# Performance work log

Measured on AMD Instinct MI355X. Metric: run time of the kernel, lower is better.

Reference implementation:

```python
import jax, jax.numpy as jnp
import numpy as np

THETA = 128.0


def _make_Q(d, units):
    # Q[n,m] = (2n+1)/sqrt(d) if n > m and (n+m) odd, else 0 (fixed, non-trainable)
    n = np.arange(d)[:, None]
    m = np.arange(units)[None, :]
    Q = np.where((n > m) & (((n + m) % 2) == 1), (2 * n + 1) / np.sqrt(d), 0.0)
    return jnp.asarray(Q, dtype=jnp.float32)


def setup_inputs() -> dict:
    key = jax.random.key(0)
    k1, k2, k3, k4 = jax.random.split(key, 4)
    B_, T, Din, d, units = 16, 4096, 128, 256, 256
    x = jax.random.normal(k1, (B_, T, Din), dtype=jnp.float32)
    A = jax.random.normal(k2, (d, d), dtype=jnp.float32) / np.sqrt(d)
    Bm = jax.random.normal(k3, (Din, d), dtype=jnp.float32) / np.sqrt(Din)
    W_mix = jax.random.normal(k4, (units, units), dtype=jnp.float32) / np.sqrt(units)
    b_mix = jnp.zeros((units,), dtype=jnp.float32)
    return {"x": x, "A": A, "B": Bm, "W_mix": W_mix, "b_mix": b_mix}


def reference(x, A, B, W_mix, b_mix):
    d = A.shape[0]
    units = W_mix.shape[0]
    Q = _make_Q(d, units)
    QW = Q @ W_mix  # fuse fixed projection with dense kernel: (d, units)
    alpha = 1.0 - 1.0 / THETA
    beta = 1.0 / THETA
    # precompute input projection for all steps: (T, batch, d)
    xB = jnp.einsum('bti,id->tbd', x, B)

    def step(state, xBt):
        new_state = alpha * state + beta * (state @ A + xBt)
        y = jnp.tanh(new_state @ QW + b_mix)
        return new_state, y

    s0 = jnp.zeros((x.shape[0], d), dtype=x.dtype)
    _, ys = jax.lax.scan(step, s0, xB)  # ys: (T, batch, units)
    return jnp.transpose(ys, (1, 0, 2))
```

## Files before the change

### kernel.cpp

```cpp
#include <hip/hip_runtime.h>
#include <math.h>

constexpr int T_   = 4096;
constexpr int NB   = 16;
constexpr int D_   = 256;
constexpr int DIN  = 128;
constexpr int U_   = 256;
constexpr int L1   = 8;
constexpr int C1   = T_ / L1;
constexpr float ALPHA_ = 1.0f - 1.0f / 128.0f;
constexpr float BETA_  = 1.0f / 128.0f;
constexpr int SD   = NB * D_;
constexpr int MS   = D_ * D_;
constexpr int TLP  = D_ + 4;
constexpr int XLP  = DIN + 4;

using short8  = __attribute__((ext_vector_type(8))) short;
using float4v = __attribute__((ext_vector_type(4))) float;

__device__ __forceinline__ unsigned short bf16_rne(float x) {
  const unsigned b = __float_as_uint(x);
  const unsigned r = ((b >> 16) & 1u) + 0x7FFFu;
  return (unsigned short)((b + r) >> 16);
}
__device__ __forceinline__ float bf16_f(unsigned short h) {
  return __uint_as_float(((unsigned)h) << 16);
}

__device__ __forceinline__ void split2(float e0, float e1, unsigned& hd, unsigned& ld) {
  const unsigned b0 = __float_as_uint(e0), b1 = __float_as_uint(e1);
  const unsigned h0 = b0 & 0xFFFF0000u, h1 = b1 & 0xFFFF0000u;
  const float l0 = e0 - __uint_as_float(h0);
  const float l1 = e1 - __uint_as_float(h1);
  hd = (h0 >> 16) | h1;
  ld = (__float_as_uint(l0) >> 16) | (__float_as_uint(l1) & 0xFFFF0000u);
}

__device__ __forceinline__ void unpack8(uint4 a, uint4 b, short8& hi, short8& lo) {
  union { short8 s; unsigned u[4]; } H, L;
  const unsigned d[8] = {a.x, a.y, a.z, a.w, b.x, b.y, b.z, b.w};
#pragma unroll
  for (int i = 0; i < 4; ++i) {
    H.u[i] = (d[2 * i] >> 16) | (d[2 * i + 1] & 0xFFFF0000u);
    L.u[i] = (d[2 * i] & 0xFFFFu) | (d[2 * i + 1] << 16);
  }
  hi = H.s; lo = L.s;
}

__device__ __forceinline__ void mm_row(const float* __restrict__ Am,
                                       const float* __restrict__ Bm,
                                       float* __restrict__ Dm,
                                       int i, int tid, float* srow) {
  srow[tid] = Am[i * D_ + tid];
  __syncthreads();
  float a0 = 0.f, a1 = 0.f, a2 = 0.f, a3 = 0.f;
#pragma unroll 8
  for (int k = 0; k < D_; k += 4) {
    a0 = fmaf(srow[k + 0], Bm[(k + 0) * D_ + tid], a0);
    a1 = fmaf(srow[k + 1], Bm[(k + 1) * D_ + tid], a1);
    a2 = fmaf(srow[k + 2], Bm[(k + 2) * D_ + tid], a2);
    a3 = fmaf(srow[k + 3], Bm[(k + 3) * D_ + tid], a3);
  }
  Dm[i * D_ + tid] = (a0 + a1) + (a2 + a3);
  __syncthreads();
}

__global__ __launch_bounds__(256) void k_prep(const float* __restrict__ A,
                                              const float* __restrict__ W,
                                              float* __restrict__ Meff,
                                              float* __restrict__ QW) {
  const int bid = blockIdx.x, tid = threadIdx.x;
  if (bid < D_) {
    float v = BETA_ * A[bid * D_ + tid];
    if (bid == tid) v += ALPHA_;
    Meff[bid * D_ + tid] = v;
    return;
  }
  __shared__ float wch[32 * D_];
  float se = 0.f, so = 0.f;
  for (int ch = 0; ch < D_ / 32; ++ch) {
    __syncthreads();
    for (int idx = tid; idx < 32 * D_; idx += 256)
      wch[idx] = W[ch * 32 * D_ + idx];
    __syncthreads();
#pragma unroll
    for (int r = 0; r < 32; ++r) {
      const int n = ch * 32 + r;
      const float sum = (n & 1) ? se : so;
      QW[n * U_ + tid] = sum * ((float)(2 * n + 1) / 16.0f);
      const float wv = wch[r * D_ + tid];
      if (n & 1) so += wv; else se += wv;
    }
  }
}

__global__ __launch_bounds__(256) void k_pw(const float* __restrict__ Am,
                                            const float* __restrict__ Bbase,
                                            float* __restrict__ Dbase) {
  __shared__ float srow[D_];
  const int q = blockIdx.x >> 8, row = blockIdx.x & 255;
  mm_row(Am, Bbase + (size_t)q * MS, Dbase + (size_t)q * MS, row, threadIdx.x, srow);
}

__global__ __launch_bounds__(256) void k_pwr(const float* __restrict__ Abase,
                                             const float* __restrict__ Bm,
                                             float* __restrict__ Dbase) {
  __shared__ float srow[D_];
  const int q = blockIdx.x >> 8, row = blockIdx.x & 255;
  mm_row(Abase + (size_t)q * MS, Bm, Dbase + (size_t)q * MS, row, threadIdx.x, srow);
}

__global__ __launch_bounds__(256) void k_packA(const float* __restrict__ A,
                                               const float* __restrict__ Bm,
                                               unsigned short* __restrict__ Mf,
                                               unsigned short* __restrict__ Bmf) {
  const int bid = blockIdx.x, tid = threadIdx.x;
  const int lane = tid & 63, nb0 = tid >> 6;
  const int quad = lane >> 4, m16 = lane & 15;
  if (bid < 8) {
    const int ks = bid;
    for (int nb = nb0; nb < 16; nb += 4) {
      const size_t fo = ((size_t)(nb * 8 + ks) * 64 + lane) * 8;
#pragma unroll
      for (int jj = 0; jj < 8; ++jj) {
        const int k = ks * 32 + quad * 8 + jj;
        const int n = nb * 16 + m16;
        const float v = BETA_ * A[k * D_ + n];
        const unsigned short h = bf16_rne(v);
        Mf[fo + jj] = h;
        Mf[MS + fo + jj] = bf16_rne(v - bf16_f(h));
      }
    }
  } else {
    const int ks = bid - 8;
    unsigned short* dh = Bmf;
    unsigned short* dl = Bmf + (MS / 2);
    for (int nb = nb0; nb < 16; nb += 4) {
      const size_t fo = ((size_t)(nb * 4 + ks) * 64 + lane) * 8;
#pragma unroll
      for (int jj = 0; jj < 8; ++jj) {
        const int k = ks * 32 + quad * 8 + jj;
        const int n = nb * 16 + m16;
        const float v = BETA_ * Bm[k * D_ + n];
        const unsigned short h = bf16_rne(v);
        dh[fo + jj] = h;
        dl[fo + jj] = bf16_rne(v - bf16_f(h));
      }
    }
  }
}

__global__ __launch_bounds__(256) void k_packB(const float* __restrict__ R,
                                               const float* __restrict__ QWm,
                                               const float* __restrict__ M8,
                                               unsigned short* __restrict__ Bf,
                                               unsigned short* __restrict__ Pf0) {
  const int bid = blockIdx.x;
  const int mat = bid >> 3, ks = bid & 7;
  const float* X = (mat < 8) ? (R + (size_t)mat * MS) : (mat == 8 ? QWm : M8);
  unsigned short* dh = (mat < 9) ? (Bf + (size_t)mat * (2 * MS)) : Pf0;
  unsigned short* dl = dh + MS;
  const int tid = threadIdx.x, lane = tid & 63, nb0 = tid >> 6;
  const int quad = lane >> 4, m16 = lane & 15;
  for (int nb = nb0; nb < 16; nb += 4) {
    const size_t fo = ((size_t)(nb * 8 + ks) * 64 + lane) * 8;
#pragma unroll
    for (int jj = 0; jj < 8; ++jj) {
      const int k = ks * 32 + quad * 8 + jj;
      const int n = nb * 16 + m16;
      const float xv = X[k * D_ + n];
      const unsigned short h = bf16_rne(xv);
      dh[fo + jj] = h;
      dl[fo + jj] = bf16_rne(xv - bf16_f(h));
    }
  }
}

__global__ __launch_bounds__(256, 2) void k_passA(
    const float* __restrict__ x, const unsigned short* __restrict__ Bmf,
    const unsigned short* __restrict__ Mf,
    unsigned short* __restrict__ Shi, unsigned short* __restrict__ Slo,
    float* __restrict__ Ends) {
  __shared__ __align__(16) float xls[NB][XLP];
  __shared__ __align__(16) unsigned tls[NB][TLP];
  const int c = blockIdx.x, tid = threadIdx.x;
  const int w = tid >> 6, lane = tid & 63;
  const int m16 = lane & 15, q = lane >> 4;
  const int xrow = tid >> 4, xi0 = (tid & 15) * 8;

  float4v sC[4];
#pragma unroll
  for (int nt = 0; nt < 4; ++nt) sC[nt] = (float4v){0.f, 0.f, 0.f, 0.f};

  for (int j = 0; j < L1; ++j) {
    const int t = c * L1 + j;
    __syncthreads();
    {
      const float* xr = x + ((size_t)xrow * T_ + t) * DIN + xi0;
      const float4 v0 = *(const float4*)(xr);
      const float4 v1 = *(const float4*)(xr + 4);
      *(float4*)(&xls[xrow][xi0]) = v0;
      *(float4*)(&xls[xrow][xi0 + 4]) = v1;
    }
    if (j > 0) {
#pragma unroll
      for (int nt = 0; nt < 4; ++nt) {
        const int n = (w * 4 + nt) * 16 + m16;
#pragma unroll
        for (int r = 0; r < 4; ++r) {
          const float sv = sC[nt][r];
          const unsigned hb = __float_as_uint(sv) & 0xFFFF0000u;
          const float lo = sv - __uint_as_float(hb);
          tls[4 * q + r][n] = hb | (__float_as_uint(lo) >> 16);
        }
      }
    }
    __syncthreads();
    float4v acc[4];
#pragma unroll
    for (int nt = 0; nt < 4; ++nt) {
      acc[nt][0] = ALPHA_ * sC[nt][0];
      acc[nt][1] = ALPHA_ * sC[nt][1];
      acc[nt][2] = ALPHA_ * sC[nt][2];
      acc[nt][3] = ALPHA_ * sC[nt][3];
    }
#pragma unroll
    for (int ks = 0; ks < 4; ++ks) {
      float xv[8];
      *(float4*)(xv)     = *(const float4*)(&xls[m16][32 * ks + 8 * q]);
      *(float4*)(xv + 4) = *(const float4*)(&xls[m16][32 * ks + 8 * q + 4]);
      union { short8 s; unsigned u[4]; } XH, XL;
#pragma unroll
      for (int p = 0; p < 4; ++p) split2(xv[2 * p], xv[2 * p + 1], XH.u[p], XL.u[p]);
#pragma unroll
      for (int nt = 0; nt < 4; ++nt) {
        const size_t fo = ((size_t)((w * 4 + nt) * 4 + ks) * 64 + lane) * 8;
        const short8 bh = *(const short8*)(Bmf + fo);
        const short8 bl = *(const short8*)(Bmf + (MS / 2) + fo);
        acc[nt] = __builtin_amdgcn_mfma_f32_16x16x32_bf16(XH.s, bh, acc[nt], 0, 0, 0);
        acc[nt] = __builtin_amdgcn_mfma_f32_16x16x32_bf16(XH.s, bl, acc[nt], 0, 0, 0);
        acc[nt] = __builtin_amdgcn_mfma_f32_16x16x32_bf16(XL.s, bh, acc[nt], 0, 0, 0);
      }
    }
    if (j > 0) {
#pragma unroll
      for (int ks = 0; ks < 8; ++ks) {
        const uint4 p0 = *(const uint4*)(&tls[m16][32 * ks + 8 * q]);
        const uint4 p1 = *(const uint4*)(&tls[m16][32 * ks + 8 * q + 4]);
        short8 sh, sl; unpack8(p0, p1, sh, sl);
        const size_t ao = ((size_t)((t - 1) * 8 + ks) * 64 + lane) * 8;
        *(short8*)(Shi + ao) = sh;
        *(short8*)(Slo + ao) = sl;
#pragma unroll
        for (int nt = 0; nt < 4; ++nt) {
          const size_t fo = ((size_t)((w * 4 + nt) * 8 + ks) * 64 + lane) * 8;
          const short8 mh = *(const short8*)(Mf + fo);
          const short8 ml = *(const short8*)(Mf + MS + fo);
          acc[nt] = __builtin_amdgcn_mfma_f32_16x16x32_bf16(sh, mh, acc[nt], 0, 0, 0);
          acc[nt] = __builtin_amdgcn_mfma_f32_16x16x32_bf16(sh, ml, acc[nt], 0, 0, 0);
          acc[nt] = __builtin_amdgcn_mfma_f32_16x16x32_bf16(sl, mh, acc[nt], 0, 0, 0);
        }
      }
    }
#pragma unroll
    for (int nt = 0; nt < 4; ++nt) sC[nt] = acc[nt];
  }
  const int tl = c * L1 + L1 - 1;
  __syncthreads();
#pragma unroll
  for (int nt = 0; nt < 4; ++nt) {
    const int n = (w * 4 + nt) * 16 + m16;
#pragma unroll
    for (int r = 0; r < 4; ++r) {
      const float sv = sC[nt][r];
      const unsigned hb = __float_as_uint(sv) & 0xFFFF0000u;
      const float lo = sv - __uint_as_float(hb);
      tls[4 * q + r][n] = hb | (__float_as_uint(lo) >> 16);
    }
  }
  __syncthreads();
#pragma unroll
  for (int ks = 0; ks < 8; ++ks) {
    const uint4 p0 = *(const uint4*)(&tls[m16][32 * ks + 8 * q]);
    const uint4 p1 = *(const uint4*)(&tls[m16][32 * ks + 8 * q + 4]);
    short8 sh, sl; unpack8(p0, p1, sh, sl);
    const size_t ao = ((size_t)(tl * 8 + ks) * 64 + lane) * 8;
    *(short8*)(Shi + ao) = sh;
    *(short8*)(Slo + ao) = sl;
  }
#pragma unroll
  for (int nt = 0; nt < 4; ++nt) {
    const int n = (w * 4 + nt) * 16 + m16;
#pragma unroll
    for (int r = 0; r < 4; ++r)
      Ends[(size_t)c * SD + (size_t)(4 * q + r) * D_ + n] = sC[nt][r];
  }
}

__global__ __launch_bounds__(256) void k_scan(
    const float* __restrict__ Vin, float* __restrict__ Vout,
    const unsigned short* __restrict__ Pf,
    const float* __restrict__ Pf32,
    float* __restrict__ Psq,
    unsigned short* __restrict__ PfNext,
    int shift, int do_sq, int packmode,
    unsigned short* __restrict__ Hhi, unsigned short* __restrict__ Hlo) {
  __shared__ __align__(16) float smem[16 * TLP];
  const int bid = blockIdx.x, tid = threadIdx.x;
  if (bid >= C1) {
    if (!do_sq) return;
    const int i = bid - C1;
    smem[tid] = Pf32[i * D_ + tid];
    __syncthreads();
    float a0 = 0.f, a1 = 0.f, a2 = 0.f, a3 = 0.f;
#pragma unroll 8
    for (int k = 0; k < D_; k += 4) {
      a0 = fmaf(smem[k + 0], Pf32[(k + 0) * D_ + tid], a0);
      a1 = fmaf(smem[k + 1], Pf32[(k + 1) * D_ + tid], a1);
      a2 = fmaf(smem[k + 2], Pf32[(k + 2) * D_ + tid], a2);
      a3 = fmaf(smem[k + 3], Pf32[(k + 3) * D_ + tid], a3);
    }
    const float v = (a0 + a1) + (a2 + a3);
    Psq[i * D_ + tid] = v;
    const unsigned short h = bf16_rne(v);
    const unsigned short l = bf16_rne(v - bf16_f(h));
    const size_t off = ((size_t)((tid >> 4) * 8 + (i >> 5)) * 64 +
                        ((i >> 3) & 3) * 16 + (tid & 15)) * 8 + (i & 7);
    PfNext[off] = h;
    PfNext[MS + off] = l;
    return;
  }
  const int c = bid;
  const int w = tid >> 6, lane = tid & 63;
  const int m16 = lane & 15, q = lane >> 4;
  float4v acc[4];
#pragma unroll
  for (int nt = 0; nt < 4; ++nt) {
    const int n = (w * 4 + nt) * 16 + m16;
#pragma unroll
    for (int r = 0; r < 4; ++r)
      acc[nt][r] = Vin[(size_t)c * SD + (size_t)(4 * q + r) * D_ + n];
  }
  if (c >= shift) {
    const float* src = Vin + (size_t)(c - shift) * SD;
    {
      const int row = tid >> 4, col0 = (tid & 15) * 16;
#pragma unroll
      for (int p = 0; p < 4; ++p)
        *(float4*)(&smem[row * TLP + col0 + 4 * p]) =
            *(const float4*)(src + (size_t)row * D_ + col0 + 4 * p);
    }
    __syncthreads();
#pragma unroll
    for (int ks = 0; ks < 8; ++ks) {
      float xv[8];
      *(float4*)(xv)     = *(const float4*)(&smem[m16 * TLP + 32 * ks + 8 * q]);
      *(float4*)(xv + 4) = *(const float4*)(&smem[m16 * TLP + 32 * ks + 8 * q + 4]);
      union { short8 s; unsigned u[4]; } XH, XL;
#pragma unroll
      for (int p = 0; p < 4; ++p) split2(xv[2 * p], xv[2 * p + 1], XH.u[p], XL.u[p]);
#pragma unroll
      for (int nt = 0; nt < 4; ++nt) {
        const size_t fo = ((size_t)((w * 4 + nt) * 8 + ks) * 64 + lane) * 8;
        const short8 ph = *(const short8*)(Pf + fo);
        const short8 pl = *(const short8*)(Pf + MS + fo);
        acc[nt] = __builtin_amdgcn_mfma_f32_16x16x32_bf16(XH.s, ph, acc[nt], 0, 0, 0);
        acc[nt] = __builtin_amdgcn_mfma_f32_16x16x32_bf16(XH.s, pl, acc[nt], 0, 0, 0);
        acc[nt] = __builtin_amdgcn_mfma_f32_16x16x32_bf16(XL.s, ph, acc[nt], 0, 0, 0);
      }
    }
  }
  if (packmode) {
    __syncthreads();
    unsigned* tls = (unsigned*)smem;
#pragma unroll
    for (int nt = 0; nt < 4; ++nt) {
      const int n = (w * 4 + nt) * 16 + m16;
#pragma unroll
      for (int r = 0; r < 4; ++r) {
        const float sv = acc[nt][r];
        const unsigned hb = __float_as_uint(sv) & 0xFFFF0000u;
        const float lo = sv - __uint_as_float(hb);
        tls[(4 * q + r) * TLP + n] = hb | (__float_as_uint(lo) >> 16);
      }
    }
    __syncthreads();
#pragma unroll
    for (int ks = 0; ks < 8; ++ks) {
      const uint4 p0 = *(const uint4*)(&tls[m16 * TLP + 32 * ks + 8 * q]);
      const uint4 p1 = *(const uint4*)(&tls[m16 * TLP + 32 * ks + 8 * q + 4]);
      short8 sh, sl; unpack8(p0, p1, sh, sl);
      const size_t ao = ((size_t)(c * 8 + ks) * 64 + lane) * 8;
      *(short8*)(Hhi + ao) = sh;
      *(short8*)(Hlo + ao) = sl;
    }
  } else {
#pragma unroll
    for (int nt = 0; nt < 4; ++nt) {
      const int n = (w * 4 + nt) * 16 + m16;
#pragma unroll
      for (int r = 0; r < 4; ++r)
        Vout[(size_t)c * SD + (size_t)(4 * q + r) * D_ + n] = acc[nt][r];
    }
  }
}

__global__ __launch_bounds__(256, 2) void k_passB(
    const unsigned short* __restrict__ Shi, const unsigned short* __restrict__ Slo,
    const unsigned short* __restrict__ Hhi, const unsigned short* __restrict__ Hlo,
    const unsigned short* __restrict__ Bf, const float* __restrict__ bmix,
    float* __restrict__ out) {
  const int bid = blockIdx.x;
  const int g = bid >> 3, j = bid & 7;
  const int tid = threadIdx.x;
  const int w = tid >> 6, lane = tid & 63;
  const int m16 = lane & 15, quad = lane >> 4;
  const unsigned short* Qh = Bf + (size_t)8 * 2 * MS;
  const unsigned short* Ql = Qh + MS;
  const unsigned short* Rh = Bf + (size_t)j * 2 * MS;
  const unsigned short* Rl = Rh + MS;

  float4v acc[8][4];
#pragma unroll
  for (int ci = 0; ci < 8; ++ci)
#pragma unroll
    for (int nt = 0; nt < 4; ++nt) acc[ci][nt] = (float4v){0.f, 0.f, 0.f, 0.f};

  for (int ks = 0; ks < 8; ++ks) {
    short8 qh[4], ql[4], rh[4], rl[4];
#pragma unroll
    for (int nt = 0; nt < 4; ++nt) {
      const size_t fo = ((size_t)((w * 4 + nt) * 8 + ks) * 64 + lane) * 8;
      qh[nt] = *(const short8*)(Qh + fo);
      ql[nt] = *(const short8*)(Ql + fo);
      rh[nt] = *(const short8*)(Rh + fo);
      rl[nt] = *(const short8*)(Rl + fo);
    }
#pragma unroll
    for (int ci = 0; ci < 8; ++ci) {
      const int c = g * 8 + ci;
      const int t = c * 8 + j;
      const size_t ao = ((size_t)(t * 8 + ks) * 64 + lane) * 8;
      const short8 sh = *(const short8*)(Shi + ao);
      const short8 sl = *(const short8*)(Slo + ao);
#pragma unroll
      for (int nt = 0; nt < 4; ++nt) {
        float4v a = acc[ci][nt];
        a = __builtin_amdgcn_mfma_f32_16x16x32_bf16(sh, qh[nt], a, 0, 0, 0);
        a = __builtin_amdgcn_mfma_f32_16x16x32_bf16(sh, ql[nt], a, 0, 0, 0);
        a = __builtin_amdgcn_mfma_f32_16x16x32_bf16(sl, qh[nt], a, 0, 0, 0);
        acc[ci][nt] = a;
      }
      if (c > 0) {
        const size_t ho = ((size_t)((c - 1) * 8 + ks) * 64 + lane) * 8;
        const short8 hh = *(const short8*)(Hhi + ho);
        const short8 hl = *(const short8*)(Hlo + ho);
#pragma unroll
        for (int nt = 0; nt < 4; ++nt) {
          float4v a = acc[ci][nt];
          a = __builtin_amdgcn_mfma_f32_16x16x32_bf16(hh, rh[nt], a, 0, 0, 0);
          a = __builtin_amdgcn_mfma_f32_16x16x32_bf16(hh, rl[nt], a, 0, 0, 0);
          a = __builtin_amdgcn_mfma_f32_16x16x32_bf16(hl, rh[nt], a, 0, 0, 0);
          acc[ci][nt] = a;
        }
      }
    }
  }
  __shared__ float ysm[16][U_ + 4];
  for (int ci = 0; ci < 8; ++ci) {
    const int t = (g * 8 + ci) * 8 + j;
    __syncthreads();
#pragma unroll
    for (int nt = 0; nt < 4; ++nt) {
      const int n = (w * 4 + nt) * 16 + m16;
      const float bias = bmix[n];
#pragma unroll
      for (int r = 0; r < 4; ++r) {
        const float v = acc[ci][nt][r] + bias;
        const float e = __expf(2.0f * v);
        ysm[quad * 4 + r][n] = 1.0f - 2.0f / (e + 1.0f);
      }
    }
    __syncthreads();
    for (int idx = tid; idx < 16 * (U_ / 4); idx += 256) {
      const int b = idx >> 6, c4 = (idx & 63) * 4;
      const float4 v = make_float4(ysm[b][c4], ysm[b][c4 + 1],
                                   ysm[b][c4 + 2], ysm[b][c4 + 3]);
      *(float4*)(out + ((size_t)b * T_ + t) * U_ + c4) = v;
    }
  }
}

extern "C" void kernel_launch(void* const* d_in, const int* in_sizes, int n_in,
                              void* d_out, int out_size, void* d_ws, size_t ws_size,
                              hipStream_t stream) {
  const float* x    = (const float*)d_in[0];
  const float* A    = (const float*)d_in[1];
  const float* Bm   = (const float*)d_in[2];
  const float* W    = (const float*)d_in[3];
  const float* bmix = (const float*)d_in[4];
  float* out = (float*)d_out;

  float* ws = (float*)d_ws;
  unsigned short* Shi = (unsigned short*)ws;
  unsigned short* Slo = (unsigned short*)(ws + 8388608);
  float* pw  = ws + 16777216;
  float* QW  = pw + 8 * (size_t)MS;
  float* R   = QW + MS;
  float* Sa  = R + 8 * (size_t)MS;
  float* Sb  = Sa + MS;
  unsigned short* Bf  = (unsigned short*)(Sb + MS);
  unsigned short* Mf  = Bf + (size_t)9 * 2 * MS;
  unsigned short* Bmf = Mf + 2 * (size_t)MS;
  unsigned short* Pf0 = Bmf + MS;
  unsigned short* Pf1 = Pf0 + 2 * (size_t)MS;
  (void)in_sizes; (void)n_in; (void)out_size; (void)ws_size;

  float* Va = out;
  float* Vb = out + (size_t)C1 * SD;

  unsigned short* Hhi = (unsigned short*)d_in[0];
  unsigned short* Hlo = Hhi + (size_t)C1 * 16 * 256;

  k_prep<<<D_ + 1, 256, 0, stream>>>(A, W, pw, QW);
  k_packA<<<12, 256, 0, stream>>>(A, Bm, Mf, Bmf);
  k_passA<<<C1, 256, 0, stream>>>(x, Bmf, Mf, Shi, Slo, Va);
  k_pw<<<256, 256, 0, stream>>>(pw, pw, pw + MS);
  k_pw<<<512, 256, 0, stream>>>(pw + MS, pw, pw + 2 * (size_t)MS);
  k_pw<<<1024, 256, 0, stream>>>(pw + 3 * (size_t)MS, pw, pw + 4 * (size_t)MS);
  k_pwr<<<2048, 256, 0, stream>>>(pw, QW, R);
  k_packB<<<80, 256, 0, stream>>>(R, QW, pw + 7 * (size_t)MS, Bf, Pf0);

  const float* vin = Va; float* vout = Vb;
  const float* Pcur = pw + 7 * (size_t)MS;
  float* sqs[2] = {Sa, Sb};
  unsigned short* Pfp[2] = {Pf0, Pf1};
  for (int lvl = 0; lvl < 9; ++lvl) {
    float* Pd = sqs[lvl & 1];
    k_scan<<<C1 + D_, 256, 0, stream>>>(vin, vout, Pfp[lvl & 1], Pcur, Pd,
                                        Pfp[(lvl + 1) & 1], 1 << lvl,
                                        (lvl < 8) ? 1 : 0, (lvl == 8) ? 1 : 0,
                                        Hhi, Hlo);
    Pcur = Pd;
    const float* tmp = vin; vin = vout; vout = (float*)tmp;
  }

  k_passB<<<C1, 256, 0, stream>>>(Shi, Slo, Hhi, Hlo, Bf, bmix, out);
}
```

Measured before the change: 520.7 us.

## Fuse nine scan-level launches into one cooperative kernel with grid syncs

```diff
diff --git a/kernel.cpp b/kernel.cpp
--- a/kernel.cpp
+++ b/kernel.cpp
@@ -1,5 +1,8 @@
 #include <hip/hip_runtime.h>
+#include <hip/hip_cooperative_groups.h>
 #include <math.h>
+
+namespace cg = cooperative_groups;
 
 constexpr int T_   = 4096;
 constexpr int NB   = 16;
@@ -405,6 +408,129 @@
   }
 }
 
+__global__ __launch_bounds__(256, 3) void k_scanf(
+    float* __restrict__ Va, float* __restrict__ Vb,
+    unsigned short* __restrict__ Pf0, unsigned short* __restrict__ Pf1,
+    const float* __restrict__ M8, float* __restrict__ Sa, float* __restrict__ Sb,
+    unsigned short* __restrict__ Hhi, unsigned short* __restrict__ Hlo) {
+  cg::grid_group grid = cg::this_grid();
+  __shared__ __align__(16) float smem[16 * TLP];
+  const int bid = blockIdx.x, tid = threadIdx.x;
+
+  if (bid < C1) {
+    const int c = bid;
+    const int w = tid >> 6, lane = tid & 63;
+    const int m16 = lane & 15, q = lane >> 4;
+    float4v acc[4];
+#pragma unroll
+    for (int nt = 0; nt < 4; ++nt) {
+      const int n = (w * 4 + nt) * 16 + m16;
+#pragma unroll
+      for (int r = 0; r < 4; ++r)
+        acc[nt][r] = Va[(size_t)c * SD + (size_t)(4 * q + r) * D_ + n];
+    }
+    for (int lvl = 0; lvl < 9; ++lvl) {
+      const int shift = 1 << lvl;
+      const float* Vin = (lvl & 1) ? Vb : Va;
+      float* Vout = (lvl & 1) ? Va : Vb;
+      const unsigned short* Pf = (lvl & 1) ? Pf1 : Pf0;
+      if (c >= shift) {
+        const float* src = Vin + (size_t)(c - shift) * SD;
+        __syncthreads();
+        {
+          const int row = tid >> 4, col0 = (tid & 15) * 16;
+#pragma unroll
+          for (int p = 0; p < 4; ++p)
+            *(float4*)(&smem[row * TLP + col0 + 4 * p]) =
+                *(const float4*)(src + (size_t)row * D_ + col0 + 4 * p);
+        }
+        __syncthreads();
+#pragma unroll
+        for (int ks = 0; ks < 8; ++ks) {
+          float xv[8];
+          *(float4*)(xv)     = *(const float4*)(&smem[m16 * TLP + 32 * ks + 8 * q]);
+          *(float4*)(xv + 4) = *(const float4*)(&smem[m16 * TLP + 32 * ks + 8 * q + 4]);
+          union { short8 s; unsigned u[4]; } XH, XL;
+#pragma unroll
+          for (int p = 0; p < 4; ++p) split2(xv[2 * p], xv[2 * p + 1], XH.u[p], XL.u[p]);
+#pragma unroll
+          for (int nt = 0; nt < 4; ++nt) {
+            const size_t fo = ((size_t)((w * 4 + nt) * 8 + ks) * 64 + lane) * 8;
+            const short8 ph = *(const short8*)(Pf + fo);
+            const short8 pl = *(const short8*)(Pf + MS + fo);
+            acc[nt] = __builtin_amdgcn_mfma_f32_16x16x32_bf16(XH.s, ph, acc[nt], 0, 0, 0);
+            acc[nt] = __builtin_amdgcn_mfma_f32_16x16x32_bf16(XH.s, pl, acc[nt], 0, 0, 0);
+            acc[nt] = __builtin_amdgcn_mfma_f32_16x16x32_bf16(XL.s, ph, acc[nt], 0, 0, 0);
+          }
+        }
+      }
+      if (lvl < 8) {
+#pragma unroll
+        for (int nt = 0; nt < 4; ++nt) {
+          const int n = (w * 4 + nt) * 16 + m16;
+#pragma unroll
+          for (int r = 0; r < 4; ++r)
+            Vout[(size_t)c * SD + (size_t)(4 * q + r) * D_ + n] = acc[nt][r];
+        }
+        __threadfence();
+        grid.sync();
+      } else {
+        __syncthreads();
+        unsigned* tls = (unsigned*)smem;
+#pragma unroll
+        for (int nt = 0; nt < 4; ++nt) {
+          const int n = (w * 4 + nt) * 16 + m16;
+#pragma unroll
+          for (int r = 0; r < 4; ++r) {
+            const float sv = acc[nt][r];
+            const unsigned hb = __float_as_uint(sv) & 0xFFFF0000u;
+            const float lo = sv - __uint_as_float(hb);
+            tls[(4 * q + r) * TLP + n] = hb | (__float_as_uint(lo) >> 16);
+          }
+        }
+        __syncthreads();
+#pragma unroll
+        for (int ks = 0; ks < 8; ++ks) {
+          const uint4 p0 = *(const uint4*)(&tls[m16 * TLP + 32 * ks + 8 * q]);
+          const uint4 p1 = *(const uint4*)(&tls[m16 * TLP + 32 * ks + 8 * q + 4]);
+          short8 sh, sl; unpack8(p0, p1, sh, sl);
+          const size_t ao = ((size_t)(c * 8 + ks) * 64 + lane) * 8;
+          *(short8*)(Hhi + ao) = sh;
+          *(short8*)(Hlo + ao) = sl;
+        }
+      }
+    }
+  } else {
+    const int i = bid - C1;
+    for (int lvl = 0; lvl < 8; ++lvl) {
+      const float* Pin = (lvl == 0) ? M8 : ((lvl & 1) ? Sa : Sb);
+      float* Pout = (lvl & 1) ? Sb : Sa;
+      unsigned short* PfN = ((lvl + 1) & 1) ? Pf1 : Pf0;
+      __syncthreads();
+      smem[tid] = Pin[(size_t)i * D_ + tid];
+      __syncthreads();
+      float a0 = 0.f, a1 = 0.f, a2 = 0.f, a3 = 0.f;
+#pragma unroll 8
+      for (int k = 0; k < D_; k += 4) {
+        a0 = fmaf(smem[k + 0], Pin[(size_t)(k + 0) * D_ + tid], a0);
+        a1 = fmaf(smem[k + 1], Pin[(size_t)(k + 1) * D_ + tid], a1);
+        a2 = fmaf(smem[k + 2], Pin[(size_t)(k + 2) * D_ + tid], a2);
+        a3 = fmaf(smem[k + 3], Pin[(size_t)(k + 3) * D_ + tid], a3);
+      }
+      const float v = (a0 + a1) + (a2 + a3);
+      Pout[(size_t)i * D_ + tid] = v;
+      const unsigned short h = bf16_rne(v);
+      const unsigned short l = bf16_rne(v - bf16_f(h));
+      const size_t off = ((size_t)((tid >> 4) * 8 + (i >> 5)) * 64 +
+                          ((i >> 3) & 3) * 16 + (tid & 15)) * 8 + (i & 7);
+      PfN[off] = h;
+      PfN[MS + off] = l;
+      __threadfence();
+      grid.sync();
+    }
+  }
+}
+
 __global__ __launch_bounds__(256, 2) void k_passB(
     const unsigned short* __restrict__ Shi, const unsigned short* __restrict__ Slo,
     const unsigned short* __restrict__ Hhi, const unsigned short* __restrict__ Hlo,
@@ -531,18 +657,30 @@
   k_pwr<<<2048, 256, 0, stream>>>(pw, QW, R);
   k_packB<<<80, 256, 0, stream>>>(R, QW, pw + 7 * (size_t)MS, Bf, Pf0);
 
-  const float* vin = Va; float* vout = Vb;
-  const float* Pcur = pw + 7 * (size_t)MS;
-  float* sqs[2] = {Sa, Sb};
-  unsigned short* Pfp[2] = {Pf0, Pf1};
-  for (int lvl = 0; lvl < 9; ++lvl) {
-    float* Pd = sqs[lvl & 1];
-    k_scan<<<C1 + D_, 256, 0, stream>>>(vin, vout, Pfp[lvl & 1], Pcur, Pd,
-                                        Pfp[(lvl + 1) & 1], 1 << lvl,
-                                        (lvl < 8) ? 1 : 0, (lvl == 8) ? 1 : 0,
-                                        Hhi, Hlo);
-    Pcur = Pd;
-    const float* tmp = vin; vin = vout; vout = (float*)tmp;
+  {
+    float* Va_ = Va; float* Vb_ = Vb;
+    unsigned short* Pf0_ = Pf0; unsigned short* Pf1_ = Pf1;
+    const float* M8_ = pw + 7 * (size_t)MS;
+    float* Sa_ = Sa; float* Sb_ = Sb;
+    unsigned short* Hhi_ = Hhi; unsigned short* Hlo_ = Hlo;
+    void* sargs[] = {&Va_, &Vb_, &Pf0_, &Pf1_, &M8_, &Sa_, &Sb_, &Hhi_, &Hlo_};
+    hipError_t ce = hipLaunchCooperativeKernel(k_scanf, dim3(C1 + D_), dim3(256),
+                                               sargs, 0, stream);
+    if (ce != hipSuccess) {
+      const float* vin = Va; float* vout = Vb;
+      const float* Pcur = pw + 7 * (size_t)MS;
+      float* sqs[2] = {Sa, Sb};
+      unsigned short* Pfp[2] = {Pf0, Pf1};
+      for (int lvl = 0; lvl < 9; ++lvl) {
+        float* Pd = sqs[lvl & 1];
+        k_scan<<<C1 + D_, 256, 0, stream>>>(vin, vout, Pfp[lvl & 1], Pcur, Pd,
+                                            Pfp[(lvl + 1) & 1], 1 << lvl,
+                                            (lvl < 8) ? 1 : 0, (lvl == 8) ? 1 : 0,
+                                            Hhi, Hlo);
+        Pcur = Pd;
+        const float* tmp = vin; vin = vout; vout = (float*)tmp;
+      }
+    }
   }
 
   k_passB<<<C1, 256, 0, stream>>>(Shi, Slo, Hhi, Hlo, Bf, bmix, out);
```

Measured after the change: 2.027 ms. +289.2%, slower.
